# Kernel tuning notes

Measured on AMD Instinct MI355X. Metric: run time of the kernel, lower is better.

The kernel has to match this reference:

```python
import jax, jax.numpy as jnp
import numpy as np

B, N, K = 2, 2048, 30          # batch, residues, neighbors
DN, DE, L = 256, 128, 3        # dim_nodes, dim_edges, num_layers
NF, EF = 12, 28                # raw node / edge feature dims
EPS = 1e-6


def _gather(h, idx):
    # h: [B,N,D], idx: [B,N,K] -> [B,N,K,D]
    b, n, k = idx.shape
    d = h.shape[-1]
    return jnp.take_along_axis(h, idx.reshape(b, n * k, 1), axis=1).reshape(b, n, k, d)


def _nrm(v):
    return v / (jnp.linalg.norm(v, axis=-1, keepdims=True) + EPS)


def _forward(X, C, Wn, bn, We, be, Wm1, bm1, Wm2, bm2, Wue1, bue1, Wue2, bue2):
    mask_i = (C > 0).astype(X.dtype)                      # [B,N]
    Nat, CA, Cat, Oat = X[..., 0, :], X[..., 1, :], X[..., 2, :], X[..., 3, :]

    # local residue frames via Gram-Schmidt on (N, CA, C)
    u = _nrm(Cat - CA)
    v0 = Nat - CA
    v = _nrm(v0 - jnp.sum(v0 * u, -1, keepdims=True) * u)
    w = jnp.cross(u, v)
    R = jnp.stack([u, v, w], axis=-1)                     # [B,N,3,3]

    # node features: internal coords (unit bond vectors + log lengths)
    def bond_feat(bv):
        return jnp.concatenate([_nrm(bv), jnp.log(jnp.linalg.norm(bv, axis=-1, keepdims=True) + EPS)], -1)
    node_feat = jnp.concatenate([bond_feat(CA - Nat), bond_feat(Cat - CA), bond_feat(Oat - Cat)], -1)  # [B,N,12]
    node_h = (node_feat @ Wn + bn) * mask_i[..., None]

    # kNN graph on centroid distances (graph_distance_atom_type=-1)
    Xc = X.mean(axis=2)                                   # [B,N,3]
    D2 = jnp.sum((Xc[:, :, None] - Xc[:, None, :]) ** 2, -1)  # [B,N,N]
    BIG = 1e9
    D2 = D2 + BIG * (1.0 - mask_i)[:, None, :] + BIG * jnp.eye(N, dtype=X.dtype)[None]
    _, edge_idx = jax.lax.top_k(-D2, K)                   # [B,N,K]

    mask_j = _gather(mask_i[..., None], edge_idx)[..., 0]
    mask_ij = mask_i[..., None] * mask_j                  # [B,N,K]

    # edge features: RBF distances + local-frame direction + relative rotation
    xj = _gather(Xc, edge_idx)
    d = xj - Xc[:, :, None]                               # [B,N,K,3]
    dist = jnp.linalg.norm(d, axis=-1)
    local = jnp.einsum('bndc,bnkd->bnkc', R, d)           # R_i^T d
    dirv = local / (dist[..., None] + EPS)
    Rj = _gather(R.reshape(B, N, 9), edge_idx).reshape(B, N, K, 3, 3)
    Rrel = jnp.einsum('bnde,bnkdf->bnkef', R, Rj).reshape(B, N, K, 9)  # R_i^T R_j
    centers = jnp.linspace(0.0, 20.0, 16)
    sigma = 20.0 / 16.0
    rbf = jnp.exp(-(((dist[..., None] - centers) / sigma) ** 2))       # [B,N,K,16]
    edge_h = (jnp.concatenate([rbf, dirv, Rrel], -1) @ We + be) * mask_ij[..., None]

    # GNN message passing: gather -> MLP -> masked mean scatter, + edge update
    denom = jnp.sum(mask_ij, -1, keepdims=True) + EPS     # [B,N,1]
    for l in range(L):
        hj = _gather(node_h, edge_idx)                    # [B,N,K,DN]
        hi = jnp.broadcast_to(node_h[:, :, None], hj.shape)
        mi = jnp.concatenate([hi, hj, edge_h], -1)        # [B,N,K,2*DN+DE]
        m = jax.nn.softplus(mi @ Wm1[l] + bm1[l]) @ Wm2[l] + bm2[l]
        m = m * mask_ij[..., None]
        node_h = (node_h + m.sum(axis=2) / denom) * mask_i[..., None]
        e = jax.nn.softplus(mi @ Wue1[l] + bue1[l]) @ Wue2[l] + bue2[l]
        edge_h = (edge_h + e) * mask_ij[..., None]

    return node_h, edge_h, edge_idx, mask_i, mask_ij


def setup_inputs() -> dict:
    key = jax.random.key(0)
    ks = jax.random.split(key, 10)
    s = lambda i, shp: jax.random.normal(ks[i], shp, jnp.float32) * 0.05
    M = 2 * DN + DE
    inp = {
        'X': jax.random.normal(ks[0], (B, N, 4, 3), jnp.float32),
        'C': jax.random.randint(ks[1], (B, N), 0, 4),
        'Wn': s(2, (NF, DN)), 'bn': jnp.zeros((DN,), jnp.float32),
        'We': s(3, (EF, DE)), 'be': jnp.zeros((DE,), jnp.float32),
        'Wm1': s(4, (L, M, DN)), 'bm1': jnp.zeros((L, DN), jnp.float32),
        'Wm2': s(5, (L, DN, DN)), 'bm2': jnp.zeros((L, DN), jnp.float32),
        'Wue1': s(6, (L, M, DE)), 'bue1': jnp.zeros((L, DE), jnp.float32),
        'Wue2': s(7, (L, DE, DE)), 'bue2': jnp.zeros((L, DE), jnp.float32),
    }
    return inp


def reference(X, C, Wn, bn, We, be, Wm1, bm1, Wm2, bm2, Wue1, bue1, Wue2, bue2):
    return _forward(X, C, Wn, bn, We, be, Wm1, bm1, Wm2, bm2, Wue1, bue1, Wue2, bue2)
```

## Files before the change

### kernel.cpp

```cpp
#include <hip/hip_runtime.h>
#include <math.h>

#define Bdim 2
#define Nn   2048
#define Kn   30
#define KP   32
#define DNc  256
#define DEc  128
#define NODES (Bdim*Nn)
#define EDGES (Bdim*Nn*Kn)
#define RPAD  (NODES*KP)
#define EPSF 1e-6f

#define BK 64
#define LDA (BK+8)
#define LDA0 40
#define LDP 136

typedef __attribute__((ext_vector_type(8))) short short8;
typedef __attribute__((ext_vector_type(4))) short sh4;
typedef __attribute__((ext_vector_type(4))) float floatx4;

__device__ __forceinline__ float softplusf(float x){
    float e = __expf(-fabsf(x));
// ... 171 lines not shown
    float* __restrict__ mask_ij_out, float* __restrict__ mask_pad,
    int* __restrict__ jg_pad, float* __restrict__ cnt)
{
    int r   = blockIdx.x*256 + threadIdx.x;
    int nid = r >> 5;
    int k   = r & 31;
    int b   = nid >> 11;
    float mij = 0.f;
    int   jb  = nid;
    float f[28];
    if (k < Kn){
        int e = nid*Kn + k;
        int j = eidx[e];
        jb = (b<<11) + j;
        mij = (C[nid] > 0 && C[jb] > 0) ? 1.f : 0.f;
        mask_ij_out[e] = mij;
        float xi0 = Xc[nid*3+0], xi1 = Xc[nid*3+1], xi2 = Xc[nid*3+2];
        float d0  = Xc[jb*3+0]-xi0;
        float d1  = Xc[jb*3+1]-xi1;
        float d2v = Xc[jb*3+2]-xi2;
        float dist = sqrtf(d0*d0 + d1*d1 + d2v*d2v);
        float ri[9], rj[9];
        #pragma unroll
        for (int q=0;q<9;++q) ri[q] = Rm[nid*9+q];
        #pragma unroll
        for (int q=0;q<9;++q) rj[q] = Rm[jb*9+q];
        #pragma unroll
        for (int c=0; c<16; ++c){
            float ctr = (20.f/15.f)*(float)c;
            float t = (dist - ctr)*(1.f/1.25f);
            f[c] = expf(-t*t);
        }
        #pragma unroll
        for (int cc=0; cc<3; ++cc){
            float loc = ri[0*3+cc]*d0 + ri[1*3+cc]*d1 + ri[2*3+cc]*d2v;
            f[16+cc] = loc/(dist+EPSF);
        }
        #pragma unroll
        for (int ee=0; ee<3; ++ee)
            #pragma unroll
            for (int ff=0; ff<3; ++ff)
                f[19+ee*3+ff] = ri[0+ee]*rj[0+ff] + ri[3+ee]*rj[3+ff] + ri[6+ee]*rj[6+ff];
    }
    jg_pad[r]   = jb;
    mask_pad[r] = mij;

    unsigned long long bal = __ballot(mij > 0.f);
    int lane = threadIdx.x & 63;
    if (lane == 0)  cnt[r >> 5] = (float)__popcll(bal & 0xFFFFFFFFull);
    if (lane == 32) cnt[r >> 5] = (float)__popcll(bal >> 32);

    unsigned short ov[32];
    #pragma unroll
    for (int q=0;q<32;++q) ov[q] = 0;
    if (k < Kn){
        #pragma unroll
        for (int q=0;q<28;++q) ov[q] = f2bf(f[q]);
    }
    unsigned short* dst = featp + (size_t)r*32;
    #pragma unroll
    for (int q=0; q<4; ++q){
        short8 sv;
        #pragma unroll
        for (int z=0; z<8; ++z) sv[z] = (short)ov[q*8+z];
        *(short8*)(dst + q*8) = sv;
    }
}

__global__ __launch_bounds__(256) void k_edge0(
    const unsigned short* __restrict__ featp, const unsigned short* __restrict__ Wp,
    const float* __restrict__ be, const float* __restrict__ mask_pad,
    unsigned short* __restrict__ edge_pad)
{
    __shared__ __align__(16) unsigned short smem[128*LDP];
    __shared__ float smask[128];
    unsigned short* Als  = smem;
    unsigned short* Bls  = smem + 128*LDA0;
    unsigned short* tile = smem;

    int tid = threadIdx.x;
    int lane = tid & 63, wave = tid >> 6;
    int wm = wave >> 1, wn = wave & 1;

    {
        const unsigned short* Ab = featp + (size_t)blockIdx.x*128*32;
        #pragma unroll
        for (int it=0; it<2; ++it){
            int idx = it*256 + tid;
            int row = idx >> 2, q = idx & 3;
            *(float4*)(&Als[row*LDA0 + q*8]) = *(const float4*)(Ab + row*32 + q*8);
        }
        if (tid < 128){
            int row = tid;
            *(float4*)(&Bls[row*LDA0 + 0])  = *(const float4*)(Wp + row*32 + 0);
            *(float4*)(&Bls[row*LDA0 + 8])  = *(const float4*)(Wp + row*32 + 8);
            *(float4*)(&Bls[row*LDA0 + 16]) = *(const float4*)(Wp + row*32 + 16);
            *(float4*)(&Bls[row*LDA0 + 24]) = *(const float4*)(Wp + row*32 + 24);
        } else {
            smask[tid-128] = mask_pad[blockIdx.x*128 + (tid-128)];
        }
    }
    __syncthreads();

    floatx4 acc[4][4];
    #pragma unroll
    for (int i=0;i<4;++i)
        #pragma unroll
        for (int j=0;j<4;++j) acc[i][j] = (floatx4){0.f,0.f,0.f,0.f};
    short8 af[4], bf[4];
    int kidx = (lane>>4)*8;
    #pragma unroll
    for (int t=0;t<4;++t){
        int row = wm*64 + t*16 + (lane&15);
        af[t] = *(const short8*)(&Als[row*LDA0 + kidx]);
        int col = wn*64 + t*16 + (lane&15);
        bf[t] = *(const short8*)(&Bls[col*LDA0 + kidx]);
    }
    __syncthreads();
    #pragma unroll
    for (int i=0;i<4;++i)
        #pragma unroll
        for (int j=0;j<4;++j)
            acc[i][j] = __builtin_amdgcn_mfma_f32_16x16x32_bf16(bf[j], af[i], acc[i][j], 0,0,0);

    int quad = lane >> 4, cl = lane & 15;
    #pragma unroll
    for (int i=0;i<4;++i){
        int rowl = wm*64 + i*16 + cl;
        float mk = smask[rowl];
        #pragma unroll
        for (int j=0;j<4;++j){
            int coll = wn*64 + j*16 + quad*4;
            float4 bv = *(const float4*)&be[coll];
            sh4 w;
            w[0] = (short)f2bf((acc[i][j][0] + bv.x)*mk);
            w[1] = (short)f2bf((acc[i][j][1] + bv.y)*mk);
            w[2] = (short)f2bf((acc[i][j][2] + bv.z)*mk);
            w[3] = (short)f2bf((acc[i][j][3] + bv.w)*mk);
            *(sh4*)(&tile[rowl*LDP + coll]) = w;
        }
    }
    __syncthreads();
    {
        int rl = tid >> 1;
        int h  = tid & 1;
        unsigned short* dst = edge_pad + (size_t)(blockIdx.x*128 + rl)*128 + h*64;
        #pragma unroll
        for (int q=0; q<8; ++q)
            *(short8*)(dst + q*8) = *(const short8*)(&tile[rl*LDP + h*64 + q*8]);
    }
}

__global__ __launch_bounds__(256) void k_pack_all(
    const float* __restrict__ We, const float* __restrict__ Wm1,
    const float* __restrict__ Wue1, const float* __restrict__ Wue2,
    const float* __restrict__ Wm2,
    unsigned short* __restrict__ wWe0, unsigned short* __restrict__ wPQw,
    unsigned short* __restrict__ wEw, unsigned short* __restrict__ wUe2w,
    unsigned short* __restrict__ wM2w)
{
    int id = blockIdx.x*256 + threadIdx.x;
    if (id < 4096){
        int n = id >> 5, kk = id & 31;
        wWe0[id] = (kk < 28) ? f2bf(We[kk*128 + n]) : 0;
        return;
    }
    id -= 4096;
    if (id < 3*768*256){
        int l = id / (768*256);
        int rem = id % (768*256);
        int n = rem >> 8, k = rem & 255;
        int c = (n < 384) ? n : n - 384;
        int r = (n < 384) ? k : 256 + k;
        float v = (c < 256) ? Wm1[((size_t)l*640 + r)*256 + c]
                            : Wue1[((size_t)l*640 + r)*128 + (c-256)];
        wPQw[id] = f2bf(v);
        return;
    }
    id -= 3*768*256;
    if (id < 3*384*128){
        int l = id / (384*128);
        int rem = id % (384*128);
        int n = rem >> 7, k = rem & 127;
        int r = 512 + k;
        float v = (n < 256) ? Wm1[((size_t)l*640 + r)*256 + n]
                            : Wue1[((size_t)l*640 + r)*128 + (n-256)];
        wEw[id] = f2bf(v);
        return;
    }
    id -= 3*384*128;
    if (id < 3*128*128){
        int l = id / (128*128);
        int rem = id % (128*128);
        int n = rem >> 7, k = rem & 127;
        wUe2w[id] = f2bf(Wue2[((size_t)l*128 + k)*128 + n]);
        return;
    }
    id -= 3*128*128;
    if (id < 3*256*256){
        int l = id / (256*256);
        int rem = id % (256*256);
        int n = rem >> 8, k = rem & 255;
        wM2w[id] = f2bf(Wm2[((size_t)l*256 + k)*256 + n]);
    }
}

template<int NR>
__device__ __forceinline__ void stage_tile_t(
    const unsigned short* __restrict__ gbase, int ldg, int k0,
    unsigned short* lds, int tid)
{
    #pragma unroll
    for (int it=0; it<NR/32; ++it){
        int idx = it*256 + tid;
        int row = idx >> 3;
        int ke  = (idx & 7) * 8;
        const float4* src = (const float4*)(gbase + (size_t)row*ldg + k0 + ke);
        *(float4*)(&lds[row*LDA + ke]) = *src;
    }
}

template<int TI, int TJ>
__device__ __forceinline__ void mma_tile_t(
    const unsigned short* Als, const unsigned short* Bls,
    int wm, int wn, int lane, floatx4 acc[TI][TJ])
{
    #pragma unroll
    for (int s=0; s<2; ++s){
        short8 af[TI], bf[TJ];
        int kidx = s*32 + (lane>>4)*8;
        #pragma unroll
        for (int t=0;t<TI;++t){
            int row = wm*(TI*16) + t*16 + (lane&15);
            af[t] = *(const short8*)(&Als[row*LDA + kidx]);
        }
        #pragma unroll
        for (int t=0;t<TJ;++t){
            int col = wn*(TJ*16) + t*16 + (lane&15);
            bf[t] = *(const short8*)(&Bls[col*LDA + kidx]);
        }
        #pragma unroll
        for (int i=0;i<TI;++i)
            #pragma unroll
            for (int j=0;j<TJ;++j)
                acc[i][j] = __builtin_amdgcn_mfma_f32_16x16x32_bf16(af[i], bf[j], acc[i][j], 0,0,0);
    }
}

template<int TI, int TJ>
__device__ __forceinline__ void mma_tile_sw(
    const unsigned short* Als, const unsigned short* Bls,
    int wm, int wn, int lane, floatx4 acc[TI][TJ])
{
    #pragma unroll
    for (int s=0; s<2; ++s){
        short8 af[TI], bf[TJ];
        int kidx = s*32 + (lane>>4)*8;
        #pragma unroll
        for (int t=0;t<TI;++t){
            int row = wm*(TI*16) + t*16 + (lane&15);
            af[t] = *(const short8*)(&Als[row*LDA + kidx]);
        }
        #pragma unroll
        for (int t=0;t<TJ;++t){
            int col = wn*(TJ*16) + t*16 + (lane&15);
            bf[t] = *(const short8*)(&Bls[col*LDA + kidx]);
        }
        #pragma unroll
        for (int i=0;i<TI;++i)
            #pragma unroll
            for (int j=0;j<TJ;++j)
                acc[i][j] = __builtin_amdgcn_mfma_f32_16x16x32_bf16(bf[j], af[i], acc[i][j], 0,0,0);
    }
}

__device__ __forceinline__ void mma_tileA_lp(
    const unsigned short* Atile, const unsigned short* Bls,
    int k0, int wm, int wn, int lane, floatx4 acc[4][4])
{
    #pragma unroll
    for (int s=0; s<2; ++s){
        short8 af[4], bf[4];
        int kloc = s*32 + (lane>>4)*8;
        #pragma unroll
        for (int t=0;t<4;++t){
            int row = wm*64 + t*16 + (lane&15);
            af[t] = *(const short8*)(&Atile[row*LDP + k0 + kloc]);
            int col = wn*64 + t*16 + (lane&15);
            bf[t] = *(const short8*)(&Bls[col*LDA + kloc]);
        }
        #pragma unroll
        for (int i=0;i<4;++i)
            #pragma unroll
            for (int j=0;j<4;++j)
                acc[i][j] = __builtin_amdgcn_mfma_f32_16x16x32_bf16(af[i], bf[j], acc[i][j], 0,0,0);
    }
}

__global__ __launch_bounds__(256) void k_pq(
    const unsigned short* __restrict__ A, const unsigned short* __restrict__ Bw,
    unsigned short* __restrict__ PQbf,
    const float* __restrict__ bm1l, const float* __restrict__ bue1l)
{
    __shared__ __align__(16) unsigned short smem[(64+128)*LDA];
    unsigned short* Als = smem;
    unsigned short* Bls = smem + 64*LDA;
    unsigned short* tile = smem;
    int tid = threadIdx.x;
    int lane = tid & 63, wave = tid >> 6;
    int wm = wave >> 1, wn = wave & 1;
    const unsigned short* Ab = A + (size_t)blockIdx.x*64*256;
    const unsigned short* Bb = Bw + (size_t)blockIdx.y*128*256;
    floatx4 acc[2][4];
    #pragma unroll
    for (int i=0;i<2;++i)
        #pragma unroll
        for (int j=0;j<4;++j) acc[i][j] = (floatx4){0.f,0.f,0.f,0.f};
    for (int k0=0; k0<256; k0+=BK){
        stage_tile_t<64>(Ab, 256, k0, Als, tid);
        stage_tile_t<128>(Bb, 256, k0, Bls, tid);
        __syncthreads();
        mma_tile_sw<2,4>(Als, Bls, wm, wn, lane, acc);
        __syncthreads();
    }
    int quad = lane >> 4, cl = lane & 15;
    #pragma unroll
    for (int i=0;i<2;++i){
        int rowl = wm*32 + i*16 + cl;
        #pragma unroll
        for (int j=0;j<4;++j){
            int coll = wn*64 + j*16 + quad*4;
            int col0 = blockIdx.y*128 + coll;
            float4 bv;
            if (col0 < 256)      bv = *(const float4*)&bm1l[col0];
            else if (col0 < 384) bv = *(const float4*)&bue1l[col0-256];
            else                 bv = (float4){0.f,0.f,0.f,0.f};
            sh4 w;
            w[0] = (short)f2bf(acc[i][j][0] + bv.x);
            w[1] = (short)f2bf(acc[i][j][1] + bv.y);
            w[2] = (short)f2bf(acc[i][j][2] + bv.z);
            w[3] = (short)f2bf(acc[i][j][3] + bv.w);
            *(sh4*)(&tile[rowl*LDP + coll]) = w;
        }
    }
    __syncthreads();
    {
        int rl = tid >> 2;
        int h  = tid & 3;
        unsigned short* dst = PQbf + (size_t)(blockIdx.x*64 + rl)*768 + blockIdx.y*128 + h*32;
        #pragma unroll
        for (int q=0; q<4; ++q)
            *(short8*)(dst + q*8) = *(const short8*)(&tile[rl*LDP + h*32 + q*8]);
    }
}

__global__ __launch_bounds__(256) void k_h1(
    const unsigned short* __restrict__ Apad,
    const unsigned short* __restrict__ BwAll,
    const unsigned short* __restrict__ BwU2,
    const unsigned short* __restrict__ PQbf, const int* __restrict__ jg_pad,
    const float* __restrict__ mask_pad, const float* __restrict__ bue2l,
    unsigned short* __restrict__ Sout,
    unsigned short* __restrict__ edge_nxt, float* __restrict__ edge_f32,
    int last)
{
    __shared__ __align__(16) unsigned short smem[26624];
    __shared__ float smask[128];

    int bid = blockIdx.x;
    int y   = bid % 3;
    int bx  = bid / 3;

    int tid = threadIdx.x;
    int lane = tid & 63, wave = tid >> 6;
    int wm = wave >> 1, wn = wave & 1;
    int quad = lane >> 4, cl = lane & 15;

    if (y < 2){
        unsigned short* Als = smem;
        unsigned short* Bls = smem + 128*LDA;
        unsigned short* pqT = smem;
        int colblk = y;

        const unsigned short* Ab = Apad + (size_t)bx*128*128;
        const unsigned short* Bb = BwAll + (size_t)colblk*128*128;
        floatx4 acc[4][4];
        #pragma unroll
        for (int i=0;i<4;++i)
            #pragma unroll
            for (int j=0;j<4;++j) acc[i][j] = (floatx4){0.f,0.f,0.f,0.f};
        for (int k0=0; k0<128; k0+=BK){
            stage_tile_t<128>(Ab, 128, k0, Als, tid);
            stage_tile_t<128>(Bb, 128, k0, Bls, tid);
            __syncthreads();
            mma_tile_t<4,4>(Als, Bls, wm, wn, lane, acc);
            __syncthreads();
        }

        {
            int colbase = colblk*128;
            #pragma unroll
            for (int it=0; it<2; ++it){
                int w    = it*256 + tid;
                int rq   = w & 31;
                int c8   = w >> 5;
                int row0 = rq*4;
                int r0   = bx*128 + row0;
                int ni   = r0 >> 5;
                int4 jg4 = *(const int4*)&jg_pad[r0];
                int colg = colbase + c8*8;
                short8 pv = *(const short8*)(PQbf + (size_t)ni*768 + colg);
                short8 q0 = *(const short8*)(PQbf + (size_t)jg4.x*768 + 384 + colg);
                short8 q1 = *(const short8*)(PQbf + (size_t)jg4.y*768 + 384 + colg);
                short8 q2 = *(const short8*)(PQbf + (size_t)jg4.z*768 + 384 + colg);
                short8 q3 = *(const short8*)(PQbf + (size_t)jg4.w*768 + 384 + colg);
                #pragma unroll
                for (int q=0; q<8; ++q){
                    float pf = bf2f((unsigned short)pv[q]);
                    sh4 ov;
                    ov[0] = (short)f2bf(pf + bf2f((unsigned short)q0[q]));
                    ov[1] = (short)f2bf(pf + bf2f((unsigned short)q1[q]));
                    ov[2] = (short)f2bf(pf + bf2f((unsigned short)q2[q]));
                    ov[3] = (short)f2bf(pf + bf2f((unsigned short)q3[q]));
                    *(sh4*)(&pqT[(c8*8 + q)*LDP + row0]) = ov;
                }
            }
            if (tid < 128) smask[tid] = mask_pad[bx*128 + tid];
        }
        __syncthreads();

        float sumA[4] = {0.f,0.f,0.f,0.f};
        float sumB[4] = {0.f,0.f,0.f,0.f};
        #pragma unroll
        for (int i=0;i<4;++i){
            int rowl0 = wm*64 + i*16 + quad*4;
            float4 mk = *(const float4*)&smask[rowl0];
            float mkv[4] = {mk.x, mk.y, mk.z, mk.w};
            #pragma unroll
            for (int j=0;j<4;++j){
                int coll = wn*64 + j*16 + cl;
                sh4 pq4 = *(const sh4*)(&pqT[coll*LDP + rowl0]);
                #pragma unroll
                for (int rg=0; rg<4; ++rg){
                    float v  = softplusf(acc[i][j][rg] + bf2f((unsigned short)pq4[rg]));
                    float mv = mkv[rg]*v;
                    if (i < 2) sumA[j] += mv; else sumB[j] += mv;
                }
            }
        }

        int nodeA = bx*4 + wm*2;
        #pragma unroll
        for (int j=0;j<4;++j){
            float a = sumA[j];
            a += __shfl_xor(a, 16, 64);
            a += __shfl_xor(a, 32, 64);
            float b = sumB[j];
            b += __shfl_xor(b, 16, 64);
            b += __shfl_xor(b, 32, 64);
            int col = colblk*128 + wn*64 + j*16 + cl;
            if (quad == 0)      Sout[(size_t)nodeA*256 + col]     = f2bf(a);
            else if (quad == 1) Sout[(size_t)(nodeA+1)*256 + col] = f2bf(b);
        }
    } else {
        unsigned short* Als  = smem;
        unsigned short* Bls  = smem + 128*LDA;
        unsigned short* tile = smem;
        unsigned short* B2   = smem + 128*LDP;
        const unsigned short* BwE = BwAll + (size_t)2*128*128;

        const unsigned short* Ab = Apad + (size_t)bx*128*128;
        floatx4 acc[4][4];
        #pragma unroll
        for (int i=0;i<4;++i)
            #pragma unroll
            for (int j=0;j<4;++j) acc[i][j] = (floatx4){0.f,0.f,0.f,0.f};
        for (int k0=0; k0<128; k0+=BK){
            stage_tile_t<128>(Ab, 128, k0, Als, tid);
            stage_tile_t<128>(BwE, 128, k0, Bls, tid);
            __syncthreads();
            mma_tile_t<4,4>(Als, Bls, wm, wn, lane, acc);
            __syncthreads();
        }

        stage_tile_t<128>(BwU2, 128, 0, B2, tid);

        {
            int rl = tid >> 1;
            int h  = tid & 1;
            int r  = bx*128 + rl;
            int ni = r >> 5;
            int jg = jg_pad[r];
            int cb = 256 + h*64;
            const unsigned short* Pr = PQbf + (size_t)ni*768 + cb;
            const unsigned short* Qr = PQbf + (size_t)jg*768 + 384 + cb;
            #pragma unroll
            for (int q=0; q<8; ++q){
                short8 pv = *(const short8*)(Pr + q*8);
                short8 qv = *(const short8*)(Qr + q*8);
                short8 ov;
                #pragma unroll
                for (int z=0; z<8; ++z)
                    ov[z] = (short)f2bf(bf2f((unsigned short)pv[z]) + bf2f((unsigned short)qv[z]));
                *(short8*)(&tile[rl*LDP + h*64 + q*8]) = ov;
            }
        }
        __syncthreads();

        #pragma unroll
        for (int i=0;i<4;++i){
            #pragma unroll
            for (int rg=0;rg<4;++rg){
                int rowl = wm*64 + i*16 + quad*4 + rg;
                #pragma unroll
                for (int j=0;j<4;++j){
                    int coll = wn*64 + j*16 + cl;
                    float pq = bf2f(tile[rowl*LDP + coll]);
                    float v  = softplusf(acc[i][j][rg] + pq);
                    tile[rowl*LDP + coll] = f2bf(v);
                }
            }
        }
        __syncthreads();

        floatx4 acc2[4][4];
        #pragma unroll
        for (int i=0;i<4;++i)
            #pragma unroll
            for (int j=0;j<4;++j) acc2[i][j] = (floatx4){0.f,0.f,0.f,0.f};
        mma_tileA_lp(tile, B2, 0, wm, wn, lane, acc2);
        __syncthreads();
        stage_tile_t<128>(BwU2, 128, 64, B2, tid);
        __syncthreads();
        mma_tileA_lp(tile, B2, 64, wm, wn, lane, acc2);
        __syncthreads();

        float* sbias = (float*)B2;
        #pragma unroll
        for (int i=0;i<4;++i){
            #pragma unroll
            for (int rg=0;rg<4;++rg){
                int rowl = wm*64 + i*16 + quad*4 + rg;
                #pragma unroll
                for (int j=0;j<4;++j){
                    int coll = wn*64 + j*16 + cl;
                    tile[rowl*LDP + coll] = f2bf(acc2[i][j][rg]);
                }
            }
        }
        if (tid < 128) sbias[tid] = bue2l[tid];
        __syncthreads();

        if (last){
            int c16  = lane & 31;
            int rsub = lane >> 5;
            #pragma unroll
            for (int step=0; step<16; ++step){
                int rowl = wave*32 + step*2 + rsub;
                int R = bx*128 + rowl;
                int k = R & (KP-1);
                if (k < Kn){
                    float mij = mask_pad[R];
                    int node = R >> 5;
                    int e = node*Kn + k;
                    sh4 ov = *(const sh4*)(Apad + (size_t)R*128 + c16*4);
                    sh4 av = *(const sh4*)(&tile[rowl*LDP + c16*4]);
                    float4 bv = *(const float4*)(&sbias[c16*4]);
                    float4 f;
                    f.x = (bf2f((unsigned short)ov[0]) + bf2f((unsigned short)av[0]) + bv.x)*mij;
                    f.y = (bf2f((unsigned short)ov[1]) + bf2f((unsigned short)av[1]) + bv.y)*mij;
                    f.z = (bf2f((unsigned short)ov[2]) + bf2f((unsigned short)av[2]) + bv.z)*mij;
                    f.w = (bf2f((unsigned short)ov[3]) + bf2f((unsigned short)av[3]) + bv.w)*mij;
                    *(float4*)(edge_f32 + (size_t)e*128 + c16*4) = f;
                }
            }
        } else {
            int c8   = lane & 15;
            int rsub = lane >> 4;
            #pragma unroll
            for (int step=0; step<8; ++step){
                int rowl = wave*32 + step*4 + rsub;
                int R = bx*128 + rowl;
                int k = R & (KP-1);
                unsigned short* ep = edge_nxt + (size_t)R*128 + c8*8;
                if (k < Kn){
                    float mij = mask_pad[R];
                    short8 ov = *(const short8*)(Apad + (size_t)R*128 + c8*8);
                    short8 av = *(const short8*)(&tile[rowl*LDP + c8*8]);
                    float4 b0 = *(const float4*)(&sbias[c8*8]);
                    float4 b1 = *(const float4*)(&sbias[c8*8 + 4]);
                    float nv[8];
                    nv[0] = (bf2f((unsigned short)ov[0]) + bf2f((unsigned short)av[0]) + b0.x)*mij;
                    nv[1] = (bf2f((unsigned short)ov[1]) + bf2f((unsigned short)av[1]) + b0.y)*mij;
                    nv[2] = (bf2f((unsigned short)ov[2]) + bf2f((unsigned short)av[2]) + b0.z)*mij;
                    nv[3] = (bf2f((unsigned short)ov[3]) + bf2f((unsigned short)av[3]) + b0.w)*mij;
                    nv[4] = (bf2f((unsigned short)ov[4]) + bf2f((unsigned short)av[4]) + b1.x)*mij;
                    nv[5] = (bf2f((unsigned short)ov[5]) + bf2f((unsigned short)av[5]) + b1.y)*mij;
                    nv[6] = (bf2f((unsigned short)ov[6]) + bf2f((unsigned short)av[6]) + b1.z)*mij;
                    nv[7] = (bf2f((unsigned short)ov[7]) + bf2f((unsigned short)av[7]) + b1.w)*mij;
                    short8 sv;
                    #pragma unroll
                    for (int z=0; z<8; ++z) sv[z] = (short)f2bf(nv[z]);
                    *(short8*)ep = sv;
                } else {
                    short8 z = {0,0,0,0,0,0,0,0};
                    *(short8*)ep = z;
                }
            }
        }
    }
}

__global__ __launch_bounds__(256) void k_node_gemm(
    const unsigned short* __restrict__ S, const unsigned short* __restrict__ Bw,
    const float* __restrict__ bm2l, const float* __restrict__ cnt,
    const float* __restrict__ mask_i,
    float* __restrict__ node_h, unsigned short* __restrict__ node_bf)
{
    __shared__ __align__(16) unsigned short Als[64*LDA];
    __shared__ __align__(16) unsigned short Bls[64*LDA];
    int tid = threadIdx.x;
    int lane = tid & 63, wave = tid >> 6;
    int wm = wave >> 1, wn = wave & 1;
    const unsigned short* Ab = S + (size_t)blockIdx.x*64*256;
    const unsigned short* Bb = Bw + (size_t)blockIdx.y*64*256;
    floatx4 acc[2][2];
    #pragma unroll
    for (int i=0;i<2;++i)
        #pragma unroll
        for (int j=0;j<2;++j) acc[i][j] = (floatx4){0.f,0.f,0.f,0.f};
    for (int k0=0; k0<256; k0+=BK){
        stage_tile_t<64>(Ab, 256, k0, Als, tid);
        stage_tile_t<64>(Bb, 256, k0, Bls, tid);
        __syncthreads();
        mma_tile_sw<2,2>(Als, Bls, wm, wn, lane, acc);
        __syncthreads();
    }
    int quad = lane >> 4, cl = lane & 15;
    #pragma unroll
    for (int i=0;i<2;++i){
        int nid = blockIdx.x*64 + wm*32 + i*16 + cl;
        float ct = cnt[nid];
        float mi = mask_i[nid];
        float dv = ct + EPSF;
        #pragma unroll
        for (int j=0;j<2;++j){
            int col = blockIdx.y*64 + wn*32 + j*16 + quad*4;
            float4 bv = *(const float4*)&bm2l[col];
            float4 nh = *(const float4*)&node_h[(size_t)nid*256 + col];
            float4 r;
            r.x = (nh.x + (acc[i][j][0] + ct*bv.x)/dv)*mi;
            r.y = (nh.y + (acc[i][j][1] + ct*bv.y)/dv)*mi;
            r.z = (nh.z + (acc[i][j][2] + ct*bv.z)/dv)*mi;
            r.w = (nh.w + (acc[i][j][3] + ct*bv.w)/dv)*mi;
            *(float4*)&node_h[(size_t)nid*256 + col] = r;
            sh4 w;
            w[0] = (short)f2bf(r.x);
            w[1] = (short)f2bf(r.y);
            w[2] = (short)f2bf(r.z);
            w[3] = (short)f2bf(r.w);
            *(sh4*)&node_bf[(size_t)nid*256 + col] = w;
        }
    }
}

extern "C" void kernel_launch(void* const* d_in, const int* in_sizes, int n_in,
                              void* d_out, int out_size, void* d_ws, size_t ws_size,
                              hipStream_t stream)
{
    (void)in_sizes; (void)n_in; (void)out_size; (void)ws_size;
    const float* X   = (const float*)d_in[0];
    const int*   C   = (const int*)  d_in[1];
    const float* Wn  = (const float*)d_in[2];
    const float* bn  = (const float*)d_in[3];
    const float* We  = (const float*)d_in[4];
    const float* be  = (const float*)d_in[5];
    const float* Wm1 = (const float*)d_in[6];
    const float* bm1 = (const float*)d_in[7];
    const float* Wm2 = (const float*)d_in[8];
    const float* bm2 = (const float*)d_in[9];
    const float* Wue1= (const float*)d_in[10];
    const float* bue1= (const float*)d_in[11];
    const float* Wue2= (const float*)d_in[12];
    const float* bue2= (const float*)d_in[13];

    float* out       = (float*)d_out;
    float* out_node  = out;
    float* out_edge  = out + 1048576;
    float* out_eidxf = out + 16777216;
    float* out_maski = out + 16900096;
    float* out_maskij= out + 16904192;

    char* wsb = (char*)d_ws;
    size_t off = 0;
    float* wXc    = (float*)(wsb + off); off += (size_t)12288*4;
    float* wR     = (float*)(wsb + off); off += (size_t)36864*4;
    float* wF     = (float*)(wsb + off); off += (size_t)49152*4;
    int*   wEidx  = (int*)  (wsb + off); off += (size_t)EDGES*4;
    int*   wJgPad = (int*)  (wsb + off); off += (size_t)RPAD*4;
    float* wMaskP = (float*)(wsb + off); off += (size_t)RPAD*4;
    float* wCnt   = (float*)(wsb + off); off += (size_t)NODES*4;
    unsigned short* wPQ      = (unsigned short*)(wsb + off); off += (size_t)NODES*768*2;
    unsigned short* wS       = (unsigned short*)(wsb + off); off += (size_t)NODES*256*2;
    unsigned short* wNodeBf  = (unsigned short*)(wsb + off); off += (size_t)NODES*256*2;
    unsigned short* wEdgePadA= (unsigned short*)(wsb + off); off += (size_t)RPAD*128*2;
    unsigned short* wEdgePadB= (unsigned short*)(wsb + off); off += (size_t)RPAD*128*2;
    unsigned short* wFeatP   = (unsigned short*)(wsb + off); off += (size_t)RPAD*32*2;
    unsigned short* wWe0     = (unsigned short*)(wsb + off); off += (size_t)128*32*2;
    unsigned short* wPQw     = (unsigned short*)(wsb + off); off += (size_t)3*768*256*2;
    unsigned short* wEw      = (unsigned short*)(wsb + off); off += (size_t)3*384*128*2;
    unsigned short* wUe2w    = (unsigned short*)(wsb + off); off += (size_t)3*128*128*2;
    unsigned short* wM2w     = (unsigned short*)(wsb + off); off += (size_t)3*256*256*2;

    unsigned short* eb[2] = { wEdgePadA, wEdgePadB };

    k_geom <<<16,    256, 0, stream>>>(X, C, wXc, wR, wF, out_maski);
    k_nodeh<<<NODES, 256, 0, stream>>>(wF, Wn, bn, C, out_node, wNodeBf);
    k_knn  <<<NODES/4, 256, 0, stream>>>(wXc, C, wEidx, out_eidxf);

    k_pack_all<<<3856, 256, 0, stream>>>(We, Wm1, Wue1, Wue2, Wm2,
                                         wWe0, wPQw, wEw, wUe2w, wM2w);
    k_edge_feat<<<RPAD/256, 256, 0, stream>>>(wXc, wR, wEidx, C, wFeatP,
                                              out_maskij, wMaskP, wJgPad, wCnt);
    k_edge0<<<RPAD/128, 256, 0, stream>>>(wFeatP, wWe0, be, wMaskP, wEdgePadA);

    for (int l=0; l<3; ++l){
        k_pq<<<dim3(64,6), 256, 0, stream>>>(wNodeBf, wPQw + (size_t)l*768*256, wPQ,
                                             bm1 + l*256, bue1 + l*128);
        k_h1<<<3*(RPAD/128), 256, 0, stream>>>(
            eb[l&1], wEw + (size_t)l*384*128, wUe2w + (size_t)l*128*128,
            wPQ, wJgPad, wMaskP, bue2 + l*128,
            wS, eb[(l+1)&1], out_edge, (l==2) ? 1 : 0);
        k_node_gemm<<<dim3(NODES/64,4), 256, 0, stream>>>(
            wS, wM2w + (size_t)l*256*256, bm2 + l*256, wCnt, out_maski,
            out_node, wNodeBf);
    }
}
```

Measured before the change: 520.2 us.

## Split fused edge-layer kernel in two and shrink tiles for more blocks

The combined k_h1 kernel, which branched on block index between message-sum and edge-update work, becomes two separate kernels, k_h1s and k_h1e. k_h1s uses a smaller shared-memory footprint, and k_h1e updates the edge buffer in place, so the ping-pong buffer is no longer needed. The k_pq and k_node_gemm tiles are halved to launch more blocks. The aim is better occupancy and load balance, at the cost of an extra launch per layer and smaller per-block MFMA tiles. The in-place update also no longer rewrites the padding rows and relies on them staying zero from k_edge0.

```diff
diff --git a/kernel.cpp b/kernel.cpp
--- a/kernel.cpp
+++ b/kernel.cpp
@@ -497,7 +497,7 @@
     unsigned short* __restrict__ PQbf,
     const float* __restrict__ bm1l, const float* __restrict__ bue1l)
 {
-    __shared__ __align__(16) unsigned short smem[(64+128)*LDA];
+    __shared__ __align__(16) unsigned short smem[2*64*LDA];
     unsigned short* Als = smem;
     unsigned short* Bls = smem + 64*LDA;
     unsigned short* tile = smem;
@@ -505,17 +505,17 @@
     int lane = tid & 63, wave = tid >> 6;
     int wm = wave >> 1, wn = wave & 1;
     const unsigned short* Ab = A + (size_t)blockIdx.x*64*256;
-    const unsigned short* Bb = Bw + (size_t)blockIdx.y*128*256;
-    floatx4 acc[2][4];
+    const unsigned short* Bb = Bw + (size_t)blockIdx.y*64*256;
+    floatx4 acc[2][2];
     #pragma unroll
     for (int i=0;i<2;++i)
         #pragma unroll
-        for (int j=0;j<4;++j) acc[i][j] = (floatx4){0.f,0.f,0.f,0.f};
+        for (int j=0;j<2;++j) acc[i][j] = (floatx4){0.f,0.f,0.f,0.f};
     for (int k0=0; k0<256; k0+=BK){
         stage_tile_t<64>(Ab, 256, k0, Als, tid);
-        stage_tile_t<128>(Bb, 256, k0, Bls, tid);
+        stage_tile_t<64>(Bb, 256, k0, Bls, tid);
         __syncthreads();
-        mma_tile_sw<2,4>(Als, Bls, wm, wn, lane, acc);
+        mma_tile_sw<2,2>(Als, Bls, wm, wn, lane, acc);
         __syncthreads();
     }
     int quad = lane >> 4, cl = lane & 15;
@@ -523,9 +523,9 @@
     for (int i=0;i<2;++i){
         int rowl = wm*32 + i*16 + cl;
         #pragma unroll
-        for (int j=0;j<4;++j){
-            int coll = wn*64 + j*16 + quad*4;
-            int col0 = blockIdx.y*128 + coll;
+        for (int j=0;j<2;++j){
+            int coll = wn*32 + j*16 + quad*4;
+            int col0 = blockIdx.y*64 + coll;
             float4 bv;
             if (col0 < 256)      bv = *(const float4*)&bm1l[col0];
             else if (col0 < 384) bv = *(const float4*)&bue1l[col0-256];
@@ -542,265 +542,264 @@
     {
         int rl = tid >> 2;
         int h  = tid & 3;
-        unsigned short* dst = PQbf + (size_t)(blockIdx.x*64 + rl)*768 + blockIdx.y*128 + h*32;
-        #pragma unroll
-        for (int q=0; q<4; ++q)
-            *(short8*)(dst + q*8) = *(const short8*)(&tile[rl*LDP + h*32 + q*8]);
-    }
-}
-
-__global__ __launch_bounds__(256) void k_h1(
-    const unsigned short* __restrict__ Apad,
-    const unsigned short* __restrict__ BwAll,
+        unsigned short* dst = PQbf + (size_t)(blockIdx.x*64 + rl)*768 + blockIdx.y*64 + h*16;
+        *(short8*)(dst + 0) = *(const short8*)(&tile[rl*LDP + h*16 + 0]);
+        *(short8*)(dst + 8) = *(const short8*)(&tile[rl*LDP + h*16 + 8]);
+    }
+}
+
+__global__ __launch_bounds__(256) void k_h1s(
+    const unsigned short* __restrict__ Apad, const unsigned short* __restrict__ Bw,
+    const unsigned short* __restrict__ PQbf, const int* __restrict__ jg_pad,
+    const float* __restrict__ mask_pad,
+    unsigned short* __restrict__ Sout)
+{
+    __shared__ __align__(16) unsigned short smem[2*128*LDA];
+    __shared__ float smask[128];
+    unsigned short* Als = smem;
+    unsigned short* Bls = smem + 128*LDA;
+    unsigned short* pqT = smem;
+
+    int tid = threadIdx.x;
+    int lane = tid & 63, wave = tid >> 6;
+    int wm = wave >> 1, wn = wave & 1;
+    int colblk = blockIdx.y;
+
+    const unsigned short* Ab = Apad + (size_t)blockIdx.x*128*128;
+    const unsigned short* Bb = Bw + (size_t)colblk*128*128;
+    floatx4 acc[4][4];
+    #pragma unroll
+    for (int i=0;i<4;++i)
+        #pragma unroll
+        for (int j=0;j<4;++j) acc[i][j] = (floatx4){0.f,0.f,0.f,0.f};
+    for (int k0=0; k0<128; k0+=BK){
+        stage_tile_t<128>(Ab, 128, k0, Als, tid);
+        stage_tile_t<128>(Bb, 128, k0, Bls, tid);
+        __syncthreads();
+        mma_tile_t<4,4>(Als, Bls, wm, wn, lane, acc);
+        __syncthreads();
+    }
+
+    {
+        int colbase = colblk*128;
+        #pragma unroll
+        for (int it=0; it<2; ++it){
+            int w    = it*256 + tid;
+            int rq   = w & 31;
+            int c8   = w >> 5;
+            int row0 = rq*4;
+            int r0   = blockIdx.x*128 + row0;
+            int ni   = r0 >> 5;
+            int4 jg4 = *(const int4*)&jg_pad[r0];
+            int colg = colbase + c8*8;
+            short8 pv = *(const short8*)(PQbf + (size_t)ni*768 + colg);
+            short8 q0 = *(const short8*)(PQbf + (size_t)jg4.x*768 + 384 + colg);
+            short8 q1 = *(const short8*)(PQbf + (size_t)jg4.y*768 + 384 + colg);
+            short8 q2 = *(const short8*)(PQbf + (size_t)jg4.z*768 + 384 + colg);
+            short8 q3 = *(const short8*)(PQbf + (size_t)jg4.w*768 + 384 + colg);
+            #pragma unroll
+            for (int q=0; q<8; ++q){
+                float pf = bf2f((unsigned short)pv[q]);
+                sh4 ov;
+                ov[0] = (short)f2bf(pf + bf2f((unsigned short)q0[q]));
+                ov[1] = (short)f2bf(pf + bf2f((unsigned short)q1[q]));
+                ov[2] = (short)f2bf(pf + bf2f((unsigned short)q2[q]));
+                ov[3] = (short)f2bf(pf + bf2f((unsigned short)q3[q]));
+                *(sh4*)(&pqT[(c8*8 + q)*LDP + row0]) = ov;
+            }
+        }
+        if (tid < 128) smask[tid] = mask_pad[blockIdx.x*128 + tid];
+    }
+    __syncthreads();
+
+    int quad = lane >> 4, cl = lane & 15;
+    float sumA[4] = {0.f,0.f,0.f,0.f};
+    float sumB[4] = {0.f,0.f,0.f,0.f};
+    #pragma unroll
+    for (int i=0;i<4;++i){
+        int rowl0 = wm*64 + i*16 + quad*4;
+        float4 mk = *(const float4*)&smask[rowl0];
+        float mkv[4] = {mk.x, mk.y, mk.z, mk.w};
+        #pragma unroll
+        for (int j=0;j<4;++j){
+            int coll = wn*64 + j*16 + cl;
+            sh4 pq4 = *(const sh4*)(&pqT[coll*LDP + rowl0]);
+            #pragma unroll
+            for (int rg=0; rg<4; ++rg){
+                float v  = softplusf(acc[i][j][rg] + bf2f((unsigned short)pq4[rg]));
+                float mv = mkv[rg]*v;
+                if (i < 2) sumA[j] += mv; else sumB[j] += mv;
+            }
+        }
+    }
+
+    int nodeA = blockIdx.x*4 + wm*2;
+    #pragma unroll
+    for (int j=0;j<4;++j){
+        float a = sumA[j];
+        a += __shfl_xor(a, 16, 64);
+        a += __shfl_xor(a, 32, 64);
+        float b = sumB[j];
+        b += __shfl_xor(b, 16, 64);
+        b += __shfl_xor(b, 32, 64);
+        int col = colblk*128 + wn*64 + j*16 + cl;
+        if (quad == 0)      Sout[(size_t)nodeA*256 + col]     = f2bf(a);
+        else if (quad == 1) Sout[(size_t)(nodeA+1)*256 + col] = f2bf(b);
+    }
+}
+
+__global__ __launch_bounds__(256) void k_h1e(
+    const unsigned short* __restrict__ Apad, const unsigned short* __restrict__ BwE,
     const unsigned short* __restrict__ BwU2,
     const unsigned short* __restrict__ PQbf, const int* __restrict__ jg_pad,
     const float* __restrict__ mask_pad, const float* __restrict__ bue2l,
-    unsigned short* __restrict__ Sout,
-    unsigned short* __restrict__ edge_nxt, float* __restrict__ edge_f32,
+    unsigned short* __restrict__ edge_pad, float* __restrict__ edge_f32,
     int last)
 {
     __shared__ __align__(16) unsigned short smem[26624];
-    __shared__ float smask[128];
-
-    int bid = blockIdx.x;
-    int y   = bid % 3;
-    int bx  = bid / 3;
+    unsigned short* Als  = smem;
+    unsigned short* Bls  = smem + 128*LDA;
+    unsigned short* tile = smem;
+    unsigned short* B2   = smem + 128*LDP;
 
     int tid = threadIdx.x;
     int lane = tid & 63, wave = tid >> 6;
     int wm = wave >> 1, wn = wave & 1;
+
+    const unsigned short* Ab = Apad + (size_t)blockIdx.x*128*128;
+    floatx4 acc[4][4];
+    #pragma unroll
+    for (int i=0;i<4;++i)
+        #pragma unroll
+        for (int j=0;j<4;++j) acc[i][j] = (floatx4){0.f,0.f,0.f,0.f};
+    for (int k0=0; k0<128; k0+=BK){
+        stage_tile_t<128>(Ab, 128, k0, Als, tid);
+        stage_tile_t<128>(BwE, 128, k0, Bls, tid);
+        __syncthreads();
+        mma_tile_t<4,4>(Als, Bls, wm, wn, lane, acc);
+        __syncthreads();
+    }
+
+    stage_tile_t<128>(BwU2, 128, 0, B2, tid);
+
+    {
+        int rl = tid >> 1;
+        int h  = tid & 1;
+        int r  = blockIdx.x*128 + rl;
+        int ni = r >> 5;
+        int jg = jg_pad[r];
+        int cb = 256 + h*64;
+        const unsigned short* Pr = PQbf + (size_t)ni*768 + cb;
+        const unsigned short* Qr = PQbf + (size_t)jg*768 + 384 + cb;
+        #pragma unroll
+        for (int q=0; q<8; ++q){
+            short8 pv = *(const short8*)(Pr + q*8);
+            short8 qv = *(const short8*)(Qr + q*8);
+            short8 ov;
+            #pragma unroll
+            for (int z=0; z<8; ++z)
+                ov[z] = (short)f2bf(bf2f((unsigned short)pv[z]) + bf2f((unsigned short)qv[z]));
+            *(short8*)(&tile[rl*LDP + h*64 + q*8]) = ov;
+        }
+    }
+    __syncthreads();
+
     int quad = lane >> 4, cl = lane & 15;
-
-    if (y < 2){
-        unsigned short* Als = smem;
-        unsigned short* Bls = smem + 128*LDA;
-        unsigned short* pqT = smem;
-        int colblk = y;
-
-        const unsigned short* Ab = Apad + (size_t)bx*128*128;
-        const unsigned short* Bb = BwAll + (size_t)colblk*128*128;
-        floatx4 acc[4][4];
-        #pragma unroll
-        for (int i=0;i<4;++i)
-            #pragma unroll
-            for (int j=0;j<4;++j) acc[i][j] = (floatx4){0.f,0.f,0.f,0.f};
-        for (int k0=0; k0<128; k0+=BK){
-            stage_tile_t<128>(Ab, 128, k0, Als, tid);
-            stage_tile_t<128>(Bb, 128, k0, Bls, tid);
-            __syncthreads();
-            mma_tile_t<4,4>(Als, Bls, wm, wn, lane, acc);
-            __syncthreads();
-        }
-
-        {
-            int colbase = colblk*128;
-            #pragma unroll
-            for (int it=0; it<2; ++it){
-                int w    = it*256 + tid;
-                int rq   = w & 31;
-                int c8   = w >> 5;
-                int row0 = rq*4;
-                int r0   = bx*128 + row0;
-                int ni   = r0 >> 5;
-                int4 jg4 = *(const int4*)&jg_pad[r0];
-                int colg = colbase + c8*8;
-                short8 pv = *(const short8*)(PQbf + (size_t)ni*768 + colg);
-                short8 q0 = *(const short8*)(PQbf + (size_t)jg4.x*768 + 384 + colg);
-                short8 q1 = *(const short8*)(PQbf + (size_t)jg4.y*768 + 384 + colg);
-                short8 q2 = *(const short8*)(PQbf + (size_t)jg4.z*768 + 384 + colg);
-                short8 q3 = *(const short8*)(PQbf + (size_t)jg4.w*768 + 384 + colg);
-                #pragma unroll
-                for (int q=0; q<8; ++q){
-                    float pf = bf2f((unsigned short)pv[q]);
-                    sh4 ov;
-                    ov[0] = (short)f2bf(pf + bf2f((unsigned short)q0[q]));
-                    ov[1] = (short)f2bf(pf + bf2f((unsigned short)q1[q]));
-                    ov[2] = (short)f2bf(pf + bf2f((unsigned short)q2[q]));
-                    ov[3] = (short)f2bf(pf + bf2f((unsigned short)q3[q]));
-                    *(sh4*)(&pqT[(c8*8 + q)*LDP + row0]) = ov;
-                }
-            }
-            if (tid < 128) smask[tid] = mask_pad[bx*128 + tid];
-        }
-        __syncthreads();
-
-        float sumA[4] = {0.f,0.f,0.f,0.f};
-        float sumB[4] = {0.f,0.f,0.f,0.f};
-        #pragma unroll
-        for (int i=0;i<4;++i){
-            int rowl0 = wm*64 + i*16 + quad*4;
-            float4 mk = *(const float4*)&smask[rowl0];
-            float mkv[4] = {mk.x, mk.y, mk.z, mk.w};
+    #pragma unroll
+    for (int i=0;i<4;++i){
+        #pragma unroll
+        for (int rg=0;rg<4;++rg){
+            int rowl = wm*64 + i*16 + quad*4 + rg;
             #pragma unroll
             for (int j=0;j<4;++j){
                 int coll = wn*64 + j*16 + cl;
-                sh4 pq4 = *(const sh4*)(&pqT[coll*LDP + rowl0]);
+                float pq = bf2f(tile[rowl*LDP + coll]);
+                float v  = softplusf(acc[i][j][rg] + pq);
+                tile[rowl*LDP + coll] = f2bf(v);
+            }
+        }
+    }
+    __syncthreads();
+
+    floatx4 acc2[4][4];
+    #pragma unroll
+    for (int i=0;i<4;++i)
+        #pragma unroll
+        for (int j=0;j<4;++j) acc2[i][j] = (floatx4){0.f,0.f,0.f,0.f};
+    mma_tileA_lp(tile, B2, 0, wm, wn, lane, acc2);
+    __syncthreads();
+    stage_tile_t<128>(BwU2, 128, 64, B2, tid);
+    __syncthreads();
+    mma_tileA_lp(tile, B2, 64, wm, wn, lane, acc2);
+    __syncthreads();
+
+    float* sbias = (float*)B2;
+    #pragma unroll
+    for (int i=0;i<4;++i){
+        #pragma unroll
+        for (int rg=0;rg<4;++rg){
+            int rowl = wm*64 + i*16 + quad*4 + rg;
+            #pragma unroll
+            for (int j=0;j<4;++j){
+                int coll = wn*64 + j*16 + cl;
+                tile[rowl*LDP + coll] = f2bf(acc2[i][j][rg]);
+            }
+        }
+    }
+    if (tid < 128) sbias[tid] = bue2l[tid];
+    __syncthreads();
+
+    if (last){
+        int c16  = lane & 31;
+        int rsub = lane >> 5;
+        #pragma unroll
+        for (int step=0; step<16; ++step){
+            int rowl = wave*32 + step*2 + rsub;
+            int R = blockIdx.x*128 + rowl;
+            int k = R & (KP-1);
+            if (k < Kn){
+                float mij = mask_pad[R];
+                int node = R >> 5;
+                int e = node*Kn + k;
+                sh4 ov = *(const sh4*)(edge_pad + (size_t)R*128 + c16*4);
+                sh4 av = *(const sh4*)(&tile[rowl*LDP + c16*4]);
+                float4 bv = *(const float4*)(&sbias[c16*4]);
+                float4 f;
+                f.x = (bf2f((unsigned short)ov[0]) + bf2f((unsigned short)av[0]) + bv.x)*mij;
+                f.y = (bf2f((unsigned short)ov[1]) + bf2f((unsigned short)av[1]) + bv.y)*mij;
+                f.z = (bf2f((unsigned short)ov[2]) + bf2f((unsigned short)av[2]) + bv.z)*mij;
+                f.w = (bf2f((unsigned short)ov[3]) + bf2f((unsigned short)av[3]) + bv.w)*mij;
+                *(float4*)(edge_f32 + (size_t)e*128 + c16*4) = f;
+            }
+        }
+    } else {
+        int c8   = lane & 15;
+        int rsub = lane >> 4;
+        #pragma unroll
+        for (int step=0; step<8; ++step){
+            int rowl = wave*32 + step*4 + rsub;
+            int R = blockIdx.x*128 + rowl;
+            int k = R & (KP-1);
+            if (k < Kn){
+                float mij = mask_pad[R];
+                unsigned short* ep = edge_pad + (size_t)R*128 + c8*8;
+                short8 ov = *(const short8*)ep;
+                short8 av = *(const short8*)(&tile[rowl*LDP + c8*8]);
+                float4 b0 = *(const float4*)(&sbias[c8*8]);
+                float4 b1 = *(const float4*)(&sbias[c8*8 + 4]);
+                float nv[8];
+                nv[0] = (bf2f((unsigned short)ov[0]) + bf2f((unsigned short)av[0]) + b0.x)*mij;
+                nv[1] = (bf2f((unsigned short)ov[1]) + bf2f((unsigned short)av[1]) + b0.y)*mij;
+                nv[2] = (bf2f((unsigned short)ov[2]) + bf2f((unsigned short)av[2]) + b0.z)*mij;
+                nv[3] = (bf2f((unsigned short)ov[3]) + bf2f((unsigned short)av[3]) + b0.w)*mij;
+                nv[4] = (bf2f((unsigned short)ov[4]) + bf2f((unsigned short)av[4]) + b1.x)*mij;
+                nv[5] = (bf2f((unsigned short)ov[5]) + bf2f((unsigned short)av[5]) + b1.y)*mij;
+                nv[6] = (bf2f((unsigned short)ov[6]) + bf2f((unsigned short)av[6]) + b1.z)*mij;
+                nv[7] = (bf2f((unsigned short)ov[7]) + bf2f((unsigned short)av[7]) + b1.w)*mij;
+                short8 sv;
                 #pragma unroll
-                for (int rg=0; rg<4; ++rg){
-                    float v  = softplusf(acc[i][j][rg] + bf2f((unsigned short)pq4[rg]));
-                    float mv = mkv[rg]*v;
-                    if (i < 2) sumA[j] += mv; else sumB[j] += mv;
-                }
-            }
-        }
-
-        int nodeA = bx*4 + wm*2;
-        #pragma unroll
-        for (int j=0;j<4;++j){
-            float a = sumA[j];
-            a += __shfl_xor(a, 16, 64);
-            a += __shfl_xor(a, 32, 64);
-            float b = sumB[j];
-            b += __shfl_xor(b, 16, 64);
-            b += __shfl_xor(b, 32, 64);
-            int col = colblk*128 + wn*64 + j*16 + cl;
-            if (quad == 0)      Sout[(size_t)nodeA*256 + col]     = f2bf(a);
-            else if (quad == 1) Sout[(size_t)(nodeA+1)*256 + col] = f2bf(b);
-        }
-    } else {
-        unsigned short* Als  = smem;
-        unsigned short* Bls  = smem + 128*LDA;
-        unsigned short* tile = smem;
-        unsigned short* B2   = smem + 128*LDP;
-        const unsigned short* BwE = BwAll + (size_t)2*128*128;
-
-        const unsigned short* Ab = Apad + (size_t)bx*128*128;
-        floatx4 acc[4][4];
-        #pragma unroll
-        for (int i=0;i<4;++i)
-            #pragma unroll
-            for (int j=0;j<4;++j) acc[i][j] = (floatx4){0.f,0.f,0.f,0.f};
-        for (int k0=0; k0<128; k0+=BK){
-            stage_tile_t<128>(Ab, 128, k0, Als, tid);
-            stage_tile_t<128>(BwE, 128, k0, Bls, tid);
-            __syncthreads();
-            mma_tile_t<4,4>(Als, Bls, wm, wn, lane, acc);
-            __syncthreads();
-        }
-
-        stage_tile_t<128>(BwU2, 128, 0, B2, tid);
-
-        {
-            int rl = tid >> 1;
-            int h  = tid & 1;
-            int r  = bx*128 + rl;
-            int ni = r >> 5;
-            int jg = jg_pad[r];
-            int cb = 256 + h*64;
-            const unsigned short* Pr = PQbf + (size_t)ni*768 + cb;
-            const unsigned short* Qr = PQbf + (size_t)jg*768 + 384 + cb;
-            #pragma unroll
-            for (int q=0; q<8; ++q){
-                short8 pv = *(const short8*)(Pr + q*8);
-                short8 qv = *(const short8*)(Qr + q*8);
-                short8 ov;
-                #pragma unroll
-                for (int z=0; z<8; ++z)
-                    ov[z] = (short)f2bf(bf2f((unsigned short)pv[z]) + bf2f((unsigned short)qv[z]));
-                *(short8*)(&tile[rl*LDP + h*64 + q*8]) = ov;
-            }
-        }
-        __syncthreads();
-
-        #pragma unroll
-        for (int i=0;i<4;++i){
-            #pragma unroll
-            for (int rg=0;rg<4;++rg){
-                int rowl = wm*64 + i*16 + quad*4 + rg;
-                #pragma unroll
-                for (int j=0;j<4;++j){
-                    int coll = wn*64 + j*16 + cl;
-                    float pq = bf2f(tile[rowl*LDP + coll]);
-                    float v  = softplusf(acc[i][j][rg] + pq);
-                    tile[rowl*LDP + coll] = f2bf(v);
-                }
-            }
-        }
-        __syncthreads();
-
-        floatx4 acc2[4][4];
-        #pragma unroll
-        for (int i=0;i<4;++i)
-            #pragma unroll
-            for (int j=0;j<4;++j) acc2[i][j] = (floatx4){0.f,0.f,0.f,0.f};
-        mma_tileA_lp(tile, B2, 0, wm, wn, lane, acc2);
-        __syncthreads();
-        stage_tile_t<128>(BwU2, 128, 64, B2, tid);
-        __syncthreads();
-        mma_tileA_lp(tile, B2, 64, wm, wn, lane, acc2);
-        __syncthreads();
-
-        float* sbias = (float*)B2;
-        #pragma unroll
-        for (int i=0;i<4;++i){
-            #pragma unroll
-            for (int rg=0;rg<4;++rg){
-                int rowl = wm*64 + i*16 + quad*4 + rg;
-                #pragma unroll
-                for (int j=0;j<4;++j){
-                    int coll = wn*64 + j*16 + cl;
-                    tile[rowl*LDP + coll] = f2bf(acc2[i][j][rg]);
-                }
-            }
-        }
-        if (tid < 128) sbias[tid] = bue2l[tid];
-        __syncthreads();
-
-        if (last){
-            int c16  = lane & 31;
-            int rsub = lane >> 5;
-            #pragma unroll
-            for (int step=0; step<16; ++step){
-                int rowl = wave*32 + step*2 + rsub;
-                int R = bx*128 + rowl;
-                int k = R & (KP-1);
-                if (k < Kn){
-                    float mij = mask_pad[R];
-                    int node = R >> 5;
-                    int e = node*Kn + k;
-                    sh4 ov = *(const sh4*)(Apad + (size_t)R*128 + c16*4);
-                    sh4 av = *(const sh4*)(&tile[rowl*LDP + c16*4]);
-                    float4 bv = *(const float4*)(&sbias[c16*4]);
-                    float4 f;
-                    f.x = (bf2f((unsigned short)ov[0]) + bf2f((unsigned short)av[0]) + bv.x)*mij;
-                    f.y = (bf2f((unsigned short)ov[1]) + bf2f((unsigned short)av[1]) + bv.y)*mij;
-                    f.z = (bf2f((unsigned short)ov[2]) + bf2f((unsigned short)av[2]) + bv.z)*mij;
-                    f.w = (bf2f((unsigned short)ov[3]) + bf2f((unsigned short)av[3]) + bv.w)*mij;
-                    *(float4*)(edge_f32 + (size_t)e*128 + c16*4) = f;
-                }
-            }
-        } else {
-            int c8   = lane & 15;
-            int rsub = lane >> 4;
-            #pragma unroll
-            for (int step=0; step<8; ++step){
-                int rowl = wave*32 + step*4 + rsub;
-                int R = bx*128 + rowl;
-                int k = R & (KP-1);
-                unsigned short* ep = edge_nxt + (size_t)R*128 + c8*8;
-                if (k < Kn){
-                    float mij = mask_pad[R];
-                    short8 ov = *(const short8*)(Apad + (size_t)R*128 + c8*8);
-                    short8 av = *(const short8*)(&tile[rowl*LDP + c8*8]);
-                    float4 b0 = *(const float4*)(&sbias[c8*8]);
-                    float4 b1 = *(const float4*)(&sbias[c8*8 + 4]);
-                    float nv[8];
-                    nv[0] = (bf2f((unsigned short)ov[0]) + bf2f((unsigned short)av[0]) + b0.x)*mij;
-                    nv[1] = (bf2f((unsigned short)ov[1]) + bf2f((unsigned short)av[1]) + b0.y)*mij;
-                    nv[2] = (bf2f((unsigned short)ov[2]) + bf2f((unsigned short)av[2]) + b0.z)*mij;
-                    nv[3] = (bf2f((unsigned short)ov[3]) + bf2f((unsigned short)av[3]) + b0.w)*mij;
-                    nv[4] = (bf2f((unsigned short)ov[4]) + bf2f((unsigned short)av[4]) + b1.x)*mij;
-                    nv[5] = (bf2f((unsigned short)ov[5]) + bf2f((unsigned short)av[5]) + b1.y)*mij;
-                    nv[6] = (bf2f((unsigned short)ov[6]) + bf2f((unsigned short)av[6]) + b1.z)*mij;
-                    nv[7] = (bf2f((unsigned short)ov[7]) + bf2f((unsigned short)av[7]) + b1.w)*mij;
-                    short8 sv;
-                    #pragma unroll
-                    for (int z=0; z<8; ++z) sv[z] = (short)f2bf(nv[z]);
-                    *(short8*)ep = sv;
-                } else {
-                    short8 z = {0,0,0,0,0,0,0,0};
-                    *(short8*)ep = z;
-                }
+                for (int z=0; z<8; ++z) sv[z] = (short)f2bf(nv[z]);
+                *(short8*)ep = sv;
             }
         }
     }
@@ -812,29 +811,26 @@
     const float* __restrict__ mask_i,
     float* __restrict__ node_h, unsigned short* __restrict__ node_bf)
 {
-    __shared__ __align__(16) unsigned short Als[64*LDA];
+    __shared__ __align__(16) unsigned short Als[32*LDA];
     __shared__ __align__(16) unsigned short Bls[64*LDA];
     int tid = threadIdx.x;
     int lane = tid & 63, wave = tid >> 6;
     int wm = wave >> 1, wn = wave & 1;
-    const unsigned short* Ab = S + (size_t)blockIdx.x*64*256;
+    const unsigned short* Ab = S + (size_t)blockIdx.x*32*256;
     const unsigned short* Bb = Bw + (size_t)blockIdx.y*64*256;
-    floatx4 acc[2][2];
-    #pragma unroll
-    for (int i=0;i<2;++i)
-        #pragma unroll
-        for (int j=0;j<2;++j) acc[i][j] = (floatx4){0.f,0.f,0.f,0.f};
+    floatx4 acc[1][2];
+    acc[0][0] = (floatx4){0.f,0.f,0.f,0.f};
+    acc[0][1] = (floatx4){0.f,0.f,0.f,0.f};
     for (int k0=0; k0<256; k0+=BK){
-        stage_tile_t<64>(Ab, 256, k0, Als, tid);
+        stage_tile_t<32>(Ab, 256, k0, Als, tid);
         stage_tile_t<64>(Bb, 256, k0, Bls, tid);
         __syncthreads();
-        mma_tile_sw<2,2>(Als, Bls, wm, wn, lane, acc);
+        mma_tile_sw<1,2>(Als, Bls, wm, wn, lane, acc);
         __syncthreads();
     }
     int quad = lane >> 4, cl = lane & 15;
-    #pragma unroll
-    for (int i=0;i<2;++i){
-        int nid = blockIdx.x*64 + wm*32 + i*16 + cl;
+    {
+        int nid = blockIdx.x*32 + wm*16 + cl;
         float ct = cnt[nid];
         float mi = mask_i[nid];
         float dv = ct + EPSF;
@@ -844,10 +840,10 @@
             float4 bv = *(const float4*)&bm2l[col];
             float4 nh = *(const float4*)&node_h[(size_t)nid*256 + col];
             float4 r;
-            r.x = (nh.x + (acc[i][j][0] + ct*bv.x)/dv)*mi;
-            r.y = (nh.y + (acc[i][j][1] + ct*bv.y)/dv)*mi;
-            r.z = (nh.z + (acc[i][j][2] + ct*bv.z)/dv)*mi;
-            r.w = (nh.w + (acc[i][j][3] + ct*bv.w)/dv)*mi;
+            r.x = (nh.x + (acc[0][j][0] + ct*bv.x)/dv)*mi;
+            r.y = (nh.y + (acc[0][j][1] + ct*bv.y)/dv)*mi;
+            r.z = (nh.z + (acc[0][j][2] + ct*bv.z)/dv)*mi;
+            r.w = (nh.w + (acc[0][j][3] + ct*bv.w)/dv)*mi;
             *(float4*)&node_h[(size_t)nid*256 + col] = r;
             sh4 w;
             w[0] = (short)f2bf(r.x);
@@ -898,8 +894,7 @@
     unsigned short* wPQ      = (unsigned short*)(wsb + off); off += (size_t)NODES*768*2;
     unsigned short* wS       = (unsigned short*)(wsb + off); off += (size_t)NODES*256*2;
     unsigned short* wNodeBf  = (unsigned short*)(wsb + off); off += (size_t)NODES*256*2;
-    unsigned short* wEdgePadA= (unsigned short*)(wsb + off); off += (size_t)RPAD*128*2;
-    unsigned short* wEdgePadB= (unsigned short*)(wsb + off); off += (size_t)RPAD*128*2;
+    unsigned short* wEdgePad = (unsigned short*)(wsb + off); off += (size_t)RPAD*128*2;
     unsigned short* wFeatP   = (unsigned short*)(wsb + off); off += (size_t)RPAD*32*2;
     unsigned short* wWe0     = (unsigned short*)(wsb + off); off += (size_t)128*32*2;
     unsigned short* wPQw     = (unsigned short*)(wsb + off); off += (size_t)3*768*256*2;
@@ -907,8 +902,6 @@
     unsigned short* wUe2w    = (unsigned short*)(wsb + off); off += (size_t)3*128*128*2;
     unsigned short* wM2w     = (unsigned short*)(wsb + off); off += (size_t)3*256*256*2;
 
-    unsigned short* eb[2] = { wEdgePadA, wEdgePadB };
-
     k_geom <<<16,    256, 0, stream>>>(X, C, wXc, wR, wF, out_maski);
     k_nodeh<<<NODES, 256, 0, stream>>>(wF, Wn, bn, C, out_node, wNodeBf);
     k_knn  <<<NODES/4, 256, 0, stream>>>(wXc, C, wEidx, out_eidxf);
@@ -917,16 +910,18 @@
                                          wWe0, wPQw, wEw, wUe2w, wM2w);
     k_edge_feat<<<RPAD/256, 256, 0, stream>>>(wXc, wR, wEidx, C, wFeatP,
                                               out_maskij, wMaskP, wJgPad, wCnt);
-    k_edge0<<<RPAD/128, 256, 0, stream>>>(wFeatP, wWe0, be, wMaskP, wEdgePadA);
+    k_edge0<<<RPAD/128, 256, 0, stream>>>(wFeatP, wWe0, be, wMaskP, wEdgePad);
 
     for (int l=0; l<3; ++l){
-        k_pq<<<dim3(64,6), 256, 0, stream>>>(wNodeBf, wPQw + (size_t)l*768*256, wPQ,
-                                             bm1 + l*256, bue1 + l*128);
-        k_h1<<<3*(RPAD/128), 256, 0, stream>>>(
-            eb[l&1], wEw + (size_t)l*384*128, wUe2w + (size_t)l*128*128,
-            wPQ, wJgPad, wMaskP, bue2 + l*128,
-            wS, eb[(l+1)&1], out_edge, (l==2) ? 1 : 0);
-        k_node_gemm<<<dim3(NODES/64,4), 256, 0, stream>>>(
+        k_pq<<<dim3(64,12), 256, 0, stream>>>(wNodeBf, wPQw + (size_t)l*768*256, wPQ,
+                                              bm1 + l*256, bue1 + l*128);
+        k_h1s<<<dim3(RPAD/128,2), 256, 0, stream>>>(
+            wEdgePad, wEw + (size_t)l*384*128, wPQ, wJgPad, wMaskP, wS);
+        k_h1e<<<RPAD/128, 256, 0, stream>>>(
+            wEdgePad, wEw + (size_t)l*384*128 + (size_t)256*128,
+            wUe2w + (size_t)l*128*128, wPQ, wJgPad, wMaskP, bue2 + l*128,
+            wEdgePad, out_edge, (l==2) ? 1 : 0);
+        k_node_gemm<<<dim3(NODES/32,4), 256, 0, stream>>>(
             wS, wM2w + (size_t)l*256*256, bm2 + l*256, wCnt, out_maski,
             out_node, wNodeBf);
     }
```

After: 443.8 us, median of 2. -14.7%, faster.
